# Optimization experiments

Hardware: AMD Instinct MI355X
Metric: run time of the kernel (lower is better)

## Reference

```python
import jax, jax.numpy as jnp
import numpy as np

HIDDEN = 1024
HEADS = 16
HEAD_DIM = HIDDEN // HEADS  # 64


def setup_inputs() -> dict:
    key = jax.random.key(0)
    ks = jax.random.split(key, 5)
    B, S = 1, 4096
    inputs = jax.random.normal(ks[0], (B, S, HIDDEN), dtype=jnp.float32)
    # Xavier-uniform-ish init for square [out, in] weights (torch Linear layout)
    lim = float(np.sqrt(6.0 / (HIDDEN + HIDDEN)))
    def w(k):
        return jax.random.uniform(k, (HIDDEN, HIDDEN), jnp.float32, -lim, lim)
    return {
        "inputs": inputs,
        "Wq": w(ks[1]), "bq": jnp.zeros((HIDDEN,), jnp.float32),
        "Wk": w(ks[2]), "bk": jnp.zeros((HIDDEN,), jnp.float32),
        "Wv": w(ks[3]), "bv": jnp.zeros((HIDDEN,), jnp.float32),
        "Wo": w(ks[4]), "bo": jnp.zeros((HIDDEN,), jnp.float32),
    }


def reference(inputs, Wq, bq, Wk, bk, Wv, bv, Wo, bo):
    # Chunked online-softmax attention (causal_mask=False) is mathematically
    # identical to standard softmax multi-head attention.
    B, S, _ = inputs.shape
    def proj(W, b):
        # torch Linear: x @ W.T + b, then split heads -> [B, S, H, D]
        return (inputs @ W.T + b).reshape(B, S, HEADS, HEAD_DIM)
    q = proj(Wq, bq) / jnp.asarray(np.sqrt(HEAD_DIM), inputs.dtype)
    k = proj(Wk, bk)
    v = proj(Wv, bv)
    scores = jnp.einsum("bqhd,bkhd->bhqk", q, k)          # [B, H, S, S]
    attn = jax.nn.softmax(scores, axis=-1)
    ctx = jnp.einsum("bhqk,bkhd->bqhd", attn, v)           # [B, S, H, D]
    ctx = ctx.reshape(B, S, HIDDEN)
    return ctx @ Wo.T + bo
```

## Files before the change

kernel.cpp:

```cpp
#include <hip/hip_runtime.h>
#include <hip/hip_bf16.h>

typedef float f32x4 __attribute__((ext_vector_type(4)));
typedef float f32x16 __attribute__((ext_vector_type(16)));
typedef unsigned short u16x8 __attribute__((ext_vector_type(8)));
typedef unsigned int u32x4 __attribute__((ext_vector_type(4)));
typedef __bf16 b16x8 __attribute__((ext_vector_type(8)));

static __device__ __forceinline__ unsigned short f2bf(float f) {
    unsigned int u = __builtin_bit_cast(unsigned int, f);
    return (unsigned short)((u + 0x7fffu + ((u >> 16) & 1u)) >> 16);
}

static __device__ __forceinline__ unsigned int pkbf(float a, float b) {
    unsigned short x = __builtin_bit_cast(unsigned short, (__bf16)a);
    unsigned short y = __builtin_bit_cast(unsigned short, (__bf16)b);
    return (unsigned int)x | ((unsigned int)y << 16);
}

static __device__ __forceinline__ f32x4 mfma16(u16x8 a, u16x8 b, f32x4 c) {
    return __builtin_amdgcn_mfma_f32_16x16x32_bf16(
        __builtin_bit_cast(b16x8, a), __builtin_bit_cast(b16x8, b), c, 0, 0, 0);
}

static __device__ __forceinline__ f32x16 mfma32(u16x8 a, u16x8 b, f32x16 c) {
    return __builtin_amdgcn_mfma_f32_32x32x16_bf16(
        __builtin_bit_cast(b16x8, a), __builtin_bit_cast(b16x8, b), c, 0, 0, 0);
}

__global__ __launch_bounds__(256)
void convert_x(const float* __restrict__ x, unsigned short* __restrict__ xb)
{
    size_t i = ((size_t)blockIdx.x * 256 + threadIdx.x) * 8;
    f32x4 a = *reinterpret_cast<const f32x4*>(&x[i]);
    f32x4 b = *reinterpret_cast<const f32x4*>(&x[i + 4]);
    u16x8 r;
    r[0] = f2bf(a[0]); r[1] = f2bf(a[1]); r[2] = f2bf(a[2]); r[3] = f2bf(a[3]);
    r[4] = f2bf(b[0]); r[5] = f2bf(b[1]); r[6] = f2bf(b[2]); r[7] = f2bf(b[3]);
    *reinterpret_cast<u16x8*>(&xb[i]) = r;
}

template<bool OUT_F32>
__global__ __launch_bounds__(256)
void gemm_bf16(const unsigned short* __restrict__ A,
               const float* __restrict__ B0, const float* __restrict__ B1,
               const float* __restrict__ B2,
               const float* __restrict__ bias0, const float* __restrict__ bias1,
               const float* __restrict__ bias2,
               void* c0, void* c1, void* c2,
               int K, float scale0)
{
    __shared__ unsigned short As[128][32];
    __shared__ unsigned short Bs[128][32];
    const int t = (int)threadIdx.x;
    const int wave = t >> 6, lane = t & 63;
    const int wr = wave >> 1, wc = wave & 1;
    const int lo = lane & 15, g = lane >> 4;
    const int brow = blockIdx.y * 128, bcol = blockIdx.x * 128;
    const int w = bcol >> 10;
    const int segcol = bcol & 1023;
    const float* Bw = (w == 0) ? B0 : (w == 1) ? B1 : B2;
    const float* bi = (w == 0) ? bias0 : (w == 1) ? bias1 : bias2;
    const float scale = (w == 0) ? scale0 : 1.0f;

    const int arow0 = t >> 2, ac8 = t & 3;
    const int arow1 = (t + 256) >> 2;
    const int brow0 = t >> 3, bc4 = t & 7;

    f32x4 acc[4][4] = {};
    u16x8 aReg[2];
    f32x4 bReg[4];

    aReg[0] = *reinterpret_cast<const u16x8*>(&A[(size_t)(brow + arow0) * K + ac8 * 8]);
    aReg[1] = *reinterpret_cast<const u16x8*>(&A[(size_t)(brow + arow1) * K + ac8 * 8]);
    #pragma unroll
    for (int i = 0; i < 4; ++i)
        bReg[i] = *reinterpret_cast<const f32x4*>(
            &Bw[(size_t)(segcol + brow0 + i * 32) * K + bc4 * 4]);

    for (int kt = 0; kt < K; kt += 32) {
        __syncthreads();
        *reinterpret_cast<u16x8*>(&As[arow0][ac8 * 8]) = aReg[0];
        *reinterpret_cast<u16x8*>(&As[arow1][ac8 * 8]) = aReg[1];
        #pragma unroll
        for (int i = 0; i < 4; ++i) {
            ushort4 u;
            u.x = f2bf(bReg[i][0]); u.y = f2bf(bReg[i][1]);
            u.z = f2bf(bReg[i][2]); u.w = f2bf(bReg[i][3]);
            *reinterpret_cast<ushort4*>(&Bs[brow0 + i * 32][bc4 * 4]) = u;
        }
        __syncthreads();

        int ktn = kt + 32; if (ktn >= K) ktn = 0;
        aReg[0] = *reinterpret_cast<const u16x8*>(&A[(size_t)(brow + arow0) * K + ktn + ac8 * 8]);
        aReg[1] = *reinterpret_cast<const u16x8*>(&A[(size_t)(brow + arow1) * K + ktn + ac8 * 8]);
        #pragma unroll
        for (int i = 0; i < 4; ++i)
            bReg[i] = *reinterpret_cast<const f32x4*>(
                &Bw[(size_t)(segcol + brow0 + i * 32) * K + ktn + bc4 * 4]);

        u16x8 af[4], bf[4];
        #pragma unroll
        for (int mf = 0; mf < 4; ++mf)
            af[mf] = *reinterpret_cast<const u16x8*>(&As[wr * 64 + mf * 16 + lo][g * 8]);
        #pragma unroll
        for (int nf = 0; nf < 4; ++nf)
            bf[nf] = *reinterpret_cast<const u16x8*>(&Bs[wc * 64 + nf * 16 + lo][g * 8]);
        #pragma unroll
        for (int mf = 0; mf < 4; ++mf)
            #pragma unroll
            for (int nf = 0; nf < 4; ++nf)
                acc[mf][nf] = mfma16(af[mf], bf[nf], acc[mf][nf]);
    }

    void* cp = (w == 0) ? c0 : (w == 1) ? c1 : c2;
    #pragma unroll
    for (int nf = 0; nf < 4; ++nf) {
        int colLocal = wc * 64 + nf * 16 + lo;
        int cw = segcol + colLocal;
        float bv = bi[cw];
        if (w == 2) {
            #pragma unroll
            for (int mf = 0; mf < 4; ++mf) {
                int rowb = brow + wr * 64 + mf * 16 + g * 4;
                ushort4 u;
                u.x = f2bf(acc[mf][nf][0] + bv);
                u.y = f2bf(acc[mf][nf][1] + bv);
                u.z = f2bf(acc[mf][nf][2] + bv);
                u.w = f2bf(acc[mf][nf][3] + bv);
                *reinterpret_cast<ushort4*>(
                    &((unsigned short*)cp)[(size_t)cw * 4096 + rowb]) = u;
            }
        } else {
            #pragma unroll
            for (int mf = 0; mf < 4; ++mf) {
                #pragma unroll
                for (int j = 0; j < 4; ++j) {
                    int row = brow + wr * 64 + mf * 16 + g * 4 + j;
                    float v = (acc[mf][nf][j] + bv) * scale;
                    if constexpr (OUT_F32)
                        ((float*)cp)[(size_t)row * 1024 + cw] = v;
                    else
                        ((unsigned short*)cp)[(size_t)row * 1024 + cw] = f2bf(v);
                }
            }
        }
    }
}

__global__ __launch_bounds__(256)
void attn_kernel(const unsigned short* __restrict__ Q,
                 const unsigned short* __restrict__ Kg,
                 const unsigned short* __restrict__ VTg,
                 unsigned short* __restrict__ Ctx)
{
    __shared__ unsigned short lds[2][2][4096];
    const int t = (int)threadIdx.x;
    const int lane = t & 63;
    const int q5 = lane & 31;
    const int hi = lane >> 5;
    const int bid = (int)blockIdx.x;
    const int h = (bid & 7) | (((bid >> 3) & 1) << 3);
    const int qb = bid >> 4;
    const int hc = h * 64;
    const int qbase = qb * 128 + (t >> 6) * 32;

    const int sr = t >> 3, sch = t & 7;
    const int scol = (sch ^ (sr & 7)) * 8;
    const int sdst = sr * 64 + sch * 8;

    u16x8 qf[4];
    #pragma unroll
    for (int kf = 0; kf < 4; ++kf)
        qf[kf] = *reinterpret_cast<const u16x8*>(
            &Q[(size_t)(qbase + q5) * 1024 + hc + kf * 16 + hi * 8]);

    f32x16 o0 = {}, o1 = {};
    float m = -1e30f, lsum = 0.f;

    {
        u16x8 k0 = *reinterpret_cast<const u16x8*>(&Kg[(size_t)sr * 1024 + hc + scol]);
        u16x8 k1 = *reinterpret_cast<const u16x8*>(&Kg[(size_t)(sr + 32) * 1024 + hc + scol]);
        u16x8 v0 = *reinterpret_cast<const u16x8*>(&VTg[(size_t)(hc + sr) * 4096 + scol]);
        u16x8 v1 = *reinterpret_cast<const u16x8*>(&VTg[(size_t)(hc + sr + 32) * 4096 + scol]);
        *reinterpret_cast<u16x8*>(&lds[0][0][sdst]) = k0;
        *reinterpret_cast<u16x8*>(&lds[0][0][sdst + 32 * 64]) = k1;
        *reinterpret_cast<u16x8*>(&lds[0][1][sdst]) = v0;
        *reinterpret_cast<u16x8*>(&lds[0][1][sdst + 32 * 64]) = v1;
    }

    const int swz = q5 & 7;
    int cur = 0;

    for (int kt = 0; kt < 4096; kt += 64) {
        __syncthreads();

        const int ktn = (kt + 64) & 4095;
        u16x8 kn0 = *reinterpret_cast<const u16x8*>(&Kg[(size_t)(ktn + sr) * 1024 + hc + scol]);
        u16x8 kn1 = *reinterpret_cast<const u16x8*>(&Kg[(size_t)(ktn + sr + 32) * 1024 + hc + scol]);
        u16x8 vn0 = *reinterpret_cast<const u16x8*>(&VTg[(size_t)(hc + sr) * 4096 + ktn + scol]);
        u16x8 vn1 = *reinterpret_cast<const u16x8*>(&VTg[(size_t)(hc + sr + 32) * 4096 + ktn + scol]);

        const unsigned short* Kb = lds[cur][0];
        const unsigned short* Vb = lds[cur][1];

        f32x16 s0 = {}, s1 = {};
        #pragma unroll
        for (int kf = 0; kf < 4; ++kf) {
            int off = ((kf * 2 + hi) ^ swz) * 8;
            u16x8 ka0 = *reinterpret_cast<const u16x8*>(&Kb[q5 * 64 + off]);
            u16x8 ka1 = *reinterpret_cast<const u16x8*>(&Kb[(q5 + 32) * 64 + off]);
            s0 = mfma32(ka0, qf[kf], s0);
            s1 = mfma32(ka1, qf[kf], s1);
        }

        float mx = s0[0];
        #pragma unroll
        for (int r = 1; r < 16; ++r) mx = fmaxf(mx, s0[r]);
        #pragma unroll
        for (int r = 0; r < 16; ++r) mx = fmaxf(mx, s1[r]);
        mx = fmaxf(mx, __shfl_xor(mx, 32));

        if (!__all(mx - m <= 8.f)) {
            float mn = fmaxf(m, mx);
            float scl = __builtin_amdgcn_exp2f(m - mn);
            m = mn;
            lsum *= scl;
            #pragma unroll
            for (int r = 0; r < 16; ++r) {
                int qr = (r & 3) + 8 * (r >> 2) + 4 * hi;
                float sj = __shfl(scl, qr);
                o0[r] *= sj; o1[r] *= sj;
            }
        }

        unsigned int u0[8], u1[8];
        float ps = 0.f;
        #pragma unroll
        for (int r = 0; r < 8; ++r) {
            float e0 = __builtin_amdgcn_exp2f(s0[2 * r] - m);
            float e1 = __builtin_amdgcn_exp2f(s0[2 * r + 1] - m);
            float e2 = __builtin_amdgcn_exp2f(s1[2 * r] - m);
            float e3 = __builtin_amdgcn_exp2f(s1[2 * r + 1] - m);
            ps += (e0 + e1) + (e2 + e3);
            u0[r] = pkbf(e0, e1);
            u1[r] = pkbf(e2, e3);
        }
        ps += __shfl_xor(ps, 32);
        lsum += ps;

        u16x8 pa[4];
        #pragma unroll
        for (int b = 0; b < 2; ++b) {
            #pragma unroll
            for (int ks = 0; ks < 2; ++ks) {
                unsigned int x0 = b ? u1[4 * ks]     : u0[4 * ks];
                unsigned int x1 = b ? u1[4 * ks + 1] : u0[4 * ks + 1];
                unsigned int y0 = b ? u1[4 * ks + 2] : u0[4 * ks + 2];
                unsigned int y1 = b ? u1[4 * ks + 3] : u0[4 * ks + 3];
                unsigned int sy0 = __shfl_xor(y0, 32);
                unsigned int sx0 = __shfl_xor(x0, 32);
                unsigned int sy1 = __shfl_xor(y1, 32);
                unsigned int sx1 = __shfl_xor(x1, 32);
                u32x4 d;
                d[0] = hi ? sy0 : x0;
                d[1] = hi ? sy1 : x1;
                d[2] = hi ? y0 : sx0;
                d[3] = hi ? y1 : sx1;
                pa[2 * b + ks] = __builtin_bit_cast(u16x8, d);
            }
        }

        #pragma unroll
        for (int ks = 0; ks < 4; ++ks) {
            int off = ((ks * 2 + hi) ^ swz) * 8;
            u16x8 vb0 = *reinterpret_cast<const u16x8*>(&Vb[q5 * 64 + off]);
            u16x8 vb1 = *reinterpret_cast<const u16x8*>(&Vb[(q5 + 32) * 64 + off]);
            o0 = mfma32(pa[ks], vb0, o0);
            o1 = mfma32(pa[ks], vb1, o1);
        }

        unsigned short* Kw = lds[cur ^ 1][0];
        unsigned short* Vw = lds[cur ^ 1][1];
        *reinterpret_cast<u16x8*>(&Kw[sdst]) = kn0;
        *reinterpret_cast<u16x8*>(&Kw[sdst + 32 * 64]) = kn1;
        *reinterpret_cast<u16x8*>(&Vw[sdst]) = vn0;
        *reinterpret_cast<u16x8*>(&Vw[sdst + 32 * 64]) = vn1;
        cur ^= 1;
    }

    float linv = 1.f / lsum;
    #pragma unroll
    for (int r = 0; r < 16; ++r) {
        int qr = (r & 3) + 8 * (r >> 2) + 4 * hi;
        float lr = __shfl(linv, qr);
        size_t row = (size_t)(qbase + qr) * 1024 + hc;
        Ctx[row + q5]      = f2bf(o0[r] * lr);
        Ctx[row + 32 + q5] = f2bf(o1[r] * lr);
    }
}

extern "C" void kernel_launch(void* const* d_in, const int* in_sizes, int n_in,
                              void* d_out, int out_size, void* d_ws, size_t ws_size,
                              hipStream_t stream)
{
    const float* x  = (const float*)d_in[0];
    const float* Wq = (const float*)d_in[1];
    const float* bq = (const float*)d_in[2];
    const float* Wk = (const float*)d_in[3];
    const float* bk = (const float*)d_in[4];
    const float* Wv = (const float*)d_in[5];
    const float* bv = (const float*)d_in[6];
    const float* Wo = (const float*)d_in[7];
    const float* bo = (const float*)d_in[8];
    float* out = (float*)d_out;

    const int S = 4096, HID = 1024;
    unsigned short* xb  = (unsigned short*)d_ws;
    unsigned short* qws = xb + (size_t)S * HID;
    unsigned short* kws = qws + (size_t)S * HID;
    unsigned short* vtw = kws + (size_t)S * HID;
    unsigned short* cws = xb;

    const float qscale = 0.125f * 1.44269504088896f;

    convert_x<<<2048, 256, 0, stream>>>(x, xb);

    dim3 gq(24, 32);
    gemm_bf16<false><<<gq, 256, 0, stream>>>(xb, Wq, Wk, Wv, bq, bk, bv,
                                             qws, kws, vtw, HID, qscale);

    attn_kernel<<<512, 256, 0, stream>>>(qws, kws, vtw, cws);

    dim3 go(8, 32);
    gemm_bf16<true><<<go, 256, 0, stream>>>(cws, Wo, Wo, Wo, bo, bo, bo,
                                            out, out, out, HID, 1.0f);
}
```

Before: 197.6 us.

## Pre-convert weights to bf16, use permlane32 swap, and tune attention occupancy

Adds separate kernels that convert the four weight matrices to bf16 once per call into workspace. The GEMMs then load bf16 weight tiles directly, without per-tile fp32 loads and conversions. In attention it replaces four shfl_xor calls plus selects with two permlane32_swap ops, pairs the max reduction, and sets launch_bounds to 2 blocks per CU. This costs four extra small kernel launches and extra workspace use, and falls back to the old path when the workspace is too small.

```diff
diff --git a/kernel.cpp b/kernel.cpp
--- a/kernel.cpp
+++ b/kernel.cpp
@@ -4,6 +4,7 @@
 typedef float f32x4 __attribute__((ext_vector_type(4)));
 typedef float f32x16 __attribute__((ext_vector_type(16)));
 typedef unsigned short u16x8 __attribute__((ext_vector_type(8)));
+typedef unsigned int u32x2 __attribute__((ext_vector_type(2)));
 typedef unsigned int u32x4 __attribute__((ext_vector_type(4)));
 typedef __bf16 b16x8 __attribute__((ext_vector_type(8)));
 
@@ -40,15 +41,15 @@
     *reinterpret_cast<u16x8*>(&xb[i]) = r;
 }
 
-template<bool OUT_F32>
+template<bool OUT_F32, bool B_BF16>
 __global__ __launch_bounds__(256)
-void gemm_bf16(const unsigned short* __restrict__ A,
-               const float* __restrict__ B0, const float* __restrict__ B1,
-               const float* __restrict__ B2,
-               const float* __restrict__ bias0, const float* __restrict__ bias1,
-               const float* __restrict__ bias2,
-               void* c0, void* c1, void* c2,
-               int K, float scale0)
+void gemm_k(const unsigned short* __restrict__ A,
+            const void* __restrict__ B0v, const void* __restrict__ B1v,
+            const void* __restrict__ B2v,
+            const float* __restrict__ bias0, const float* __restrict__ bias1,
+            const float* __restrict__ bias2,
+            void* c0, void* c1, void* c2,
+            int K, float scale0)
 {
     __shared__ unsigned short As[128][32];
     __shared__ unsigned short Bs[128][32];
@@ -59,45 +60,64 @@
     const int brow = blockIdx.y * 128, bcol = blockIdx.x * 128;
     const int w = bcol >> 10;
     const int segcol = bcol & 1023;
-    const float* Bw = (w == 0) ? B0 : (w == 1) ? B1 : B2;
+    const void* Bwv = (w == 0) ? B0v : (w == 1) ? B1v : B2v;
     const float* bi = (w == 0) ? bias0 : (w == 1) ? bias1 : bias2;
     const float scale = (w == 0) ? scale0 : 1.0f;
 
-    const int arow0 = t >> 2, ac8 = t & 3;
-    const int arow1 = (t + 256) >> 2;
+    const int row0 = t >> 2, c8 = t & 3;
+    const int row1 = row0 + 64;
     const int brow0 = t >> 3, bc4 = t & 7;
 
     f32x4 acc[4][4] = {};
-    u16x8 aReg[2];
-    f32x4 bReg[4];
-
-    aReg[0] = *reinterpret_cast<const u16x8*>(&A[(size_t)(brow + arow0) * K + ac8 * 8]);
-    aReg[1] = *reinterpret_cast<const u16x8*>(&A[(size_t)(brow + arow1) * K + ac8 * 8]);
-    #pragma unroll
-    for (int i = 0; i < 4; ++i)
-        bReg[i] = *reinterpret_cast<const f32x4*>(
-            &Bw[(size_t)(segcol + brow0 + i * 32) * K + bc4 * 4]);
+    u16x8 aReg[2], bRegH[2];
+    f32x4 bRegF[4];
+
+    aReg[0] = *reinterpret_cast<const u16x8*>(&A[(size_t)(brow + row0) * K + c8 * 8]);
+    aReg[1] = *reinterpret_cast<const u16x8*>(&A[(size_t)(brow + row1) * K + c8 * 8]);
+    if constexpr (B_BF16) {
+        const unsigned short* Bp = (const unsigned short*)Bwv;
+        bRegH[0] = *reinterpret_cast<const u16x8*>(&Bp[(size_t)(segcol + row0) * K + c8 * 8]);
+        bRegH[1] = *reinterpret_cast<const u16x8*>(&Bp[(size_t)(segcol + row1) * K + c8 * 8]);
+    } else {
+        const float* Bp = (const float*)Bwv;
+        #pragma unroll
+        for (int i = 0; i < 4; ++i)
+            bRegF[i] = *reinterpret_cast<const f32x4*>(
+                &Bp[(size_t)(segcol + brow0 + i * 32) * K + bc4 * 4]);
+    }
 
     for (int kt = 0; kt < K; kt += 32) {
         __syncthreads();
-        *reinterpret_cast<u16x8*>(&As[arow0][ac8 * 8]) = aReg[0];
-        *reinterpret_cast<u16x8*>(&As[arow1][ac8 * 8]) = aReg[1];
-        #pragma unroll
-        for (int i = 0; i < 4; ++i) {
-            ushort4 u;
-            u.x = f2bf(bReg[i][0]); u.y = f2bf(bReg[i][1]);
-            u.z = f2bf(bReg[i][2]); u.w = f2bf(bReg[i][3]);
-            *reinterpret_cast<ushort4*>(&Bs[brow0 + i * 32][bc4 * 4]) = u;
+        *reinterpret_cast<u16x8*>(&As[row0][c8 * 8]) = aReg[0];
+        *reinterpret_cast<u16x8*>(&As[row1][c8 * 8]) = aReg[1];
+        if constexpr (B_BF16) {
+            *reinterpret_cast<u16x8*>(&Bs[row0][c8 * 8]) = bRegH[0];
+            *reinterpret_cast<u16x8*>(&Bs[row1][c8 * 8]) = bRegH[1];
+        } else {
+            #pragma unroll
+            for (int i = 0; i < 4; ++i) {
+                ushort4 u;
+                u.x = f2bf(bRegF[i][0]); u.y = f2bf(bRegF[i][1]);
+                u.z = f2bf(bRegF[i][2]); u.w = f2bf(bRegF[i][3]);
+                *reinterpret_cast<ushort4*>(&Bs[brow0 + i * 32][bc4 * 4]) = u;
+            }
         }
         __syncthreads();
 
         int ktn = kt + 32; if (ktn >= K) ktn = 0;
-        aReg[0] = *reinterpret_cast<const u16x8*>(&A[(size_t)(brow + arow0) * K + ktn + ac8 * 8]);
-        aReg[1] = *reinterpret_cast<const u16x8*>(&A[(size_t)(brow + arow1) * K + ktn + ac8 * 8]);
-        #pragma unroll
-        for (int i = 0; i < 4; ++i)
-            bReg[i] = *reinterpret_cast<const f32x4*>(
-                &Bw[(size_t)(segcol + brow0 + i * 32) * K + ktn + bc4 * 4]);
+        aReg[0] = *reinterpret_cast<const u16x8*>(&A[(size_t)(brow + row0) * K + ktn + c8 * 8]);
+        aReg[1] = *reinterpret_cast<const u16x8*>(&A[(size_t)(brow + row1) * K + ktn + c8 * 8]);
+        if constexpr (B_BF16) {
+            const unsigned short* Bp = (const unsigned short*)Bwv;
+            bRegH[0] = *reinterpret_cast<const u16x8*>(&Bp[(size_t)(segcol + row0) * K + ktn + c8 * 8]);
+            bRegH[1] = *reinterpret_cast<const u16x8*>(&Bp[(size_t)(segcol + row1) * K + ktn + c8 * 8]);
+        } else {
+            const float* Bp = (const float*)Bwv;
+            #pragma unroll
+            for (int i = 0; i < 4; ++i)
+                bRegF[i] = *reinterpret_cast<const f32x4*>(
+                    &Bp[(size_t)(segcol + brow0 + i * 32) * K + ktn + bc4 * 4]);
+        }
 
         u16x8 af[4], bf[4];
         #pragma unroll
@@ -148,7 +168,7 @@
     }
 }
 
-__global__ __launch_bounds__(256)
+__global__ __launch_bounds__(256, 2)
 void attn_kernel(const unsigned short* __restrict__ Q,
                  const unsigned short* __restrict__ Kg,
                  const unsigned short* __restrict__ VTg,
@@ -214,11 +234,11 @@
             s1 = mfma32(ka1, qf[kf], s1);
         }
 
-        float mx = s0[0];
-        #pragma unroll
-        for (int r = 1; r < 16; ++r) mx = fmaxf(mx, s0[r]);
-        #pragma unroll
-        for (int r = 0; r < 16; ++r) mx = fmaxf(mx, s1[r]);
+        float mx = fmaxf(s0[0], s0[1]);
+        #pragma unroll
+        for (int r = 2; r < 16; r += 2) mx = fmaxf(fmaxf(mx, s0[r]), s0[r + 1]);
+        #pragma unroll
+        for (int r = 0; r < 16; r += 2) mx = fmaxf(fmaxf(mx, s1[r]), s1[r + 1]);
         mx = fmaxf(mx, __shfl_xor(mx, 32));
 
         if (!__all(mx - m <= 8.f)) {
@@ -258,15 +278,10 @@
                 unsigned int x1 = b ? u1[4 * ks + 1] : u0[4 * ks + 1];
                 unsigned int y0 = b ? u1[4 * ks + 2] : u0[4 * ks + 2];
                 unsigned int y1 = b ? u1[4 * ks + 3] : u0[4 * ks + 3];
-                unsigned int sy0 = __shfl_xor(y0, 32);
-                unsigned int sx0 = __shfl_xor(x0, 32);
-                unsigned int sy1 = __shfl_xor(y1, 32);
-                unsigned int sx1 = __shfl_xor(x1, 32);
+                u32x2 r0 = __builtin_amdgcn_permlane32_swap(x0, y0, false, false);
+                u32x2 r1 = __builtin_amdgcn_permlane32_swap(x1, y1, false, false);
                 u32x4 d;
-                d[0] = hi ? sy0 : x0;
-                d[1] = hi ? sy1 : x1;
-                d[2] = hi ? y0 : sx0;
-                d[3] = hi ? y1 : sx1;
+                d[0] = r0[0]; d[1] = r1[0]; d[2] = r0[1]; d[3] = r1[1];
                 pa[2 * b + ks] = __builtin_bit_cast(u16x8, d);
             }
         }
@@ -323,16 +338,30 @@
     unsigned short* cws = xb;
 
     const float qscale = 0.125f * 1.44269504088896f;
+    const size_t needW = ((size_t)4 * S * HID + (size_t)4 * HID * HID) * 2;
 
     convert_x<<<2048, 256, 0, stream>>>(x, xb);
 
-    dim3 gq(24, 32);
-    gemm_bf16<false><<<gq, 256, 0, stream>>>(xb, Wq, Wk, Wv, bq, bk, bv,
-                                             qws, kws, vtw, HID, qscale);
-
-    attn_kernel<<<512, 256, 0, stream>>>(qws, kws, vtw, cws);
-
-    dim3 go(8, 32);
-    gemm_bf16<true><<<go, 256, 0, stream>>>(cws, Wo, Wo, Wo, bo, bo, bo,
-                                            out, out, out, HID, 1.0f);
-}
+    dim3 gq(24, 32), go(8, 32);
+    if (ws_size >= needW) {
+        unsigned short* wqb = vtw + (size_t)S * HID;
+        unsigned short* wkb = wqb + (size_t)HID * HID;
+        unsigned short* wvb = wkb + (size_t)HID * HID;
+        unsigned short* wob = wvb + (size_t)HID * HID;
+        convert_x<<<512, 256, 0, stream>>>(Wq, wqb);
+        convert_x<<<512, 256, 0, stream>>>(Wk, wkb);
+        convert_x<<<512, 256, 0, stream>>>(Wv, wvb);
+        convert_x<<<512, 256, 0, stream>>>(Wo, wob);
+        gemm_k<false, true><<<gq, 256, 0, stream>>>(xb, wqb, wkb, wvb, bq, bk, bv,
+                                                    qws, kws, vtw, HID, qscale);
+        attn_kernel<<<512, 256, 0, stream>>>(qws, kws, vtw, cws);
+        gemm_k<true, true><<<go, 256, 0, stream>>>(cws, wob, wob, wob, bo, bo, bo,
+                                                   out, out, out, HID, 1.0f);
+    } else {
+        gemm_k<false, false><<<gq, 256, 0, stream>>>(xb, Wq, Wk, Wv, bq, bk, bv,
+                                                     qws, kws, vtw, HID, qscale);
+        attn_kernel<<<512, 256, 0, stream>>>(qws, kws, vtw, cws);
+        gemm_k<true, false><<<go, 256, 0, stream>>>(cws, Wo, Wo, Wo, bo, bo, bo,
+                                                    out, out, out, HID, 1.0f);
+    }
+}
```

After: 186.2 us. 1.06x faster.
